# Kernel tuning notes

Hardware: AMD Instinct MI355X
Metric: run time of the kernel (lower is better)

## Reference

```python
import jax, jax.numpy as jnp
import numpy as np

DIM = 384
HEADS = 12
AGENT = 49
POOL = 7  # int(sqrt(AGENT))


def setup_inputs() -> dict:
    key = jax.random.key(0)
    ks = jax.random.split(key, 9)
    b, c, h, w = 32, DIM, 56, 56
    x = jax.random.normal(ks[0], (b, c, h, w), dtype=jnp.float32)
    qkv_w = jax.random.normal(ks[1], (c, 3 * c), dtype=jnp.float32) * 0.02
    qkv_b = jnp.zeros((3 * c,), dtype=jnp.float32)
    proj_w = jax.random.normal(ks[2], (c, c), dtype=jnp.float32) * 0.02
    proj_b = jnp.zeros((c,), dtype=jnp.float32)
    an_bias = jax.random.normal(ks[3], (HEADS, AGENT, 7, 7), dtype=jnp.float32) * 0.02
    na_bias = jax.random.normal(ks[4], (HEADS, AGENT, 7, 7), dtype=jnp.float32) * 0.02
    dwc_w = jax.random.normal(ks[5], (c, 1, 3, 3), dtype=jnp.float32) * 0.1
    dwc_b = jnp.zeros((c,), dtype=jnp.float32)
    return {"x": x, "qkv_w": qkv_w, "qkv_b": qkv_b, "proj_w": proj_w,
            "proj_b": proj_b, "an_bias": an_bias, "na_bias": na_bias,
            "dwc_w": dwc_w, "dwc_b": dwc_b}


def agent_attention(x, qkv_w, qkv_b, proj_w, proj_b, an_bias, na_bias, dwc_w, dwc_b):
    b, c, h, w = x.shape
    n = h * w
    H = HEADS
    hd = c // H
    scale = hd ** -0.5

    shortcut = x
    xf = x.reshape(b, c, n).transpose(0, 2, 1)            # [b, n, c]
    qkv = xf @ qkv_w + qkv_b                              # [b, n, 3c]
    q, k, v = jnp.split(qkv, 3, axis=-1)                  # each [b, n, c]

    # agent tokens: adaptive avg pool of q over uniform (h//POOL, w//POOL) windows
    q_img = q.reshape(b, h, w, c)
    agent = q_img.reshape(b, POOL, h // POOL, POOL, w // POOL, c).mean(axis=(2, 4))
    agent = agent.reshape(b, AGENT, c)

    # split heads -> [b, H, n, hd] / [b, H, AGENT, hd]
    qh = q.reshape(b, n, H, hd).transpose(0, 2, 1, 3)
    kh = k.reshape(b, n, H, hd).transpose(0, 2, 1, 3)
    vh = v.reshape(b, n, H, hd).transpose(0, 2, 1, 3)
    ah = agent.reshape(b, AGENT, H, hd).transpose(0, 2, 1, 3)

    # stage 1: agent tokens attend to keys (pos bias bilinearly upsampled 7x7 -> h x w)
    pb1 = jax.image.resize(an_bias, (H, AGENT, h, w), method='bilinear')
    pb1 = pb1.reshape(1, H, AGENT, n)
    agent_attn = jax.nn.softmax(
        jnp.einsum('bhad,bhnd->bhan', ah * scale, kh) + pb1, axis=-1)
    agent_v = jnp.einsum('bhan,bhnd->bhad', agent_attn, vh)  # [b, H, AGENT, hd]

    # stage 2: queries attend to agent tokens
    ab1 = jax.image.resize(na_bias, (H, AGENT, h, w), method='bilinear')
    ab1 = ab1.reshape(1, H, AGENT, n).transpose(0, 1, 3, 2)  # [1, H, n, AGENT]
    q_attn = jax.nn.softmax(
        jnp.einsum('bhnd,bhad->bhna', qh * scale, ah) + ab1, axis=-1)
    o = jnp.einsum('bhna,bhad->bhnd', q_attn, agent_v)       # [b, H, n, hd]
    o = o.transpose(0, 2, 1, 3).reshape(b, n, c)

    # depthwise 3x3 conv on v (NCHW), residual add
    v_img = v.reshape(b, h, w, c).transpose(0, 3, 1, 2)      # [b, c, h, w]
    dw = jax.lax.conv_general_dilated(
        v_img, dwc_w, window_strides=(1, 1), padding='SAME',
        feature_group_count=c, dimension_numbers=('NCHW', 'OIHW', 'NCHW'))
    dw = dw + dwc_b[None, :, None, None]
    o = o + dw.transpose(0, 2, 3, 1).reshape(b, n, c)

    o = o @ proj_w + proj_b                                  # [b, n, c]
    o = o.reshape(b, h, w, c).transpose(0, 3, 1, 2)          # [b, c, h, w]
    return shortcut * jax.nn.sigmoid(o)


def reference(x, qkv_w, qkv_b, proj_w, proj_b, an_bias, na_bias, dwc_w, dwc_b):
    return agent_attention(x, qkv_w, qkv_b, proj_w, proj_b,
                           an_bias, na_bias, dwc_w, dwc_b)
```

## Files before the change

### kernel.cpp

```cpp
#include <hip/hip_runtime.h>

#define DIM    384
#define HEADS  12
#define NPIX   3136
#define BATCH  32
#define AGENTS 49
#define HD     32

typedef unsigned short u16;
typedef unsigned int   u32;
typedef __attribute__((ext_vector_type(8))) short short8;
typedef __attribute__((ext_vector_type(4))) float f32x4;

__device__ __forceinline__ float bf2f(u16 u) { return __uint_as_float(((u32)u) << 16); }
__device__ __forceinline__ u16 f2bf(float f) {
    u32 i = __float_as_uint(f);
    u32 r = i + 0x7fffu + ((i >> 16) & 1u);
    return (u16)(r >> 16);
}

__device__ __forceinline__ void unpack_row32(const u16* p, float* f) {
    const uint4* q = (const uint4*)p;
#pragma unroll
    for (int i = 0; i < 4; i++) {
        uint4 u = q[i];
        u32 w0 = u.x, w1 = u.y, w2 = u.z, w3 = u.w;
        f[i*8+0] = __uint_as_float(w0 << 16); f[i*8+1] = __uint_as_float(w0 & 0xffff0000u);
        f[i*8+2] = __uint_as_float(w1 << 16); f[i*8+3] = __uint_as_float(w1 & 0xffff0000u);
        f[i*8+4] = __uint_as_float(w2 << 16); f[i*8+5] = __uint_as_float(w2 & 0xffff0000u);
        f[i*8+6] = __uint_as_float(w3 << 16); f[i*8+7] = __uint_as_float(w3 & 0xffff0000u);
    }
}

__global__ __launch_bounds__(256) void transpose_mat(const float* __restrict__ src, u16* __restrict__ dst,
                                                     int R, int C) {
    __shared__ u16 tile[64][65];
    int c0 = blockIdx.x * 64, r0 = blockIdx.y * 64;
    int t0 = threadIdx.x & 63, t1 = threadIdx.x >> 6;
#pragma unroll
    for (int i = 0; i < 16; i++) {
        int r = t1 + i*4;
        tile[t0][r] = f2bf(src[(size_t)(r0 + r)*C + c0 + t0]);
    }
    __syncthreads();
#pragma unroll
    for (int i = 0; i < 16; i++) {
        int c = t1 + i*4;
        dst[(size_t)(c0 + c)*R + r0 + t0] = tile[c][t0];
    }
}

__global__ __launch_bounds__(256) void upsample_bias(const float* __restrict__ src, float* __restrict__ dst) {
    int idx = blockIdx.x * 256 + threadIdx.x;
    int xo = idx % 56; int t = idx / 56;
    int yo = t % 56;   int ha = t / 56;
    float fy = yo * 0.125f - 0.4375f;
    float fx = xo * 0.125f - 0.4375f;
    float y0f = floorf(fy), x0f = floorf(fx);
    float wy = fy - y0f, wx = fx - x0f;
    int y0 = (int)y0f, x0 = (int)x0f;
    int y0c = max(y0, 0), y1c = min(y0 + 1, 6);
    int x0c = max(x0, 0), x1c = min(x0 + 1, 6);
    const float* sp = src + (size_t)ha * 49;
    float v00 = sp[y0c*7 + x0c], v01 = sp[y0c*7 + x1c];
    float v10 = sp[y1c*7 + x0c], v11 = sp[y1c*7 + x1c];
    dst[idx] = (1.f-wy)*((1.f-wx)*v00 + wx*v01) + wy*((1.f-wx)*v10 + wx*v11);
}

__global__ __launch_bounds__(256) void zero_init(float* __restrict__ p, int n) {
    int i = blockIdx.x * 256 + threadIdx.x;
    if (i < n) p[i] = 0.f;
}

__device__ __forceinline__ void mfma_tile(const short* As, const short* Bs, f32x4 acc[4][4],
                                          int wm, int wn, int quad, int lr) {
#pragma unroll
    for (int ks = 0; ks < 2; ks++) {
        int g = ks*4 + quad;
        short8 af[4], bg[4];
#pragma unroll
        for (int im = 0; im < 4; im++) {
            int r = wm*64 + im*16 + lr;
            af[im] = *(const short8*)&As[r*64 + ((g ^ (r & 7)) << 3)];
        }
#pragma unroll
        for (int in_ = 0; in_ < 4; in_++) {
            int r = wn*64 + in_*16 + lr;
            bg[in_] = *(const short8*)&Bs[r*64 + ((g ^ (r & 7)) << 3)];
        }
#pragma unroll
        for (int im = 0; im < 4; im++)
#pragma unroll
            for (int in_ = 0; in_ < 4; in_++)
                acc[im][in_] = __builtin_amdgcn_mfma_f32_16x16x32_bf16(af[im], bg[in_], acc[im][in_], 0, 0, 0);
    }
}

__global__ __launch_bounds__(256) void gemm_qkv(const float* __restrict__ x, const u16* __restrict__ Bw,
                                                const float* __restrict__ bias,
                                                u16* __restrict__ qb, u16* __restrict__ kb, u16* __restrict__ vb) {
    __shared__ __align__(16) short As[128*64];
    __shared__ __align__(16) short Bs[128*64];
    f32x4 acc[4][4] = {};
    const int n0 = blockIdx.x * 128;
    const int p0 = blockIdx.y * 128;
    const int bb = blockIdx.z;
    const int tid  = threadIdx.x;
    const int lane = tid & 63, wave = tid >> 6;
    const int wm = wave >> 1, wn = wave & 1;
    const int quad = lane >> 4, lr = lane & 15;
    const int ch_ = tid >> 2;
    const int seg = tid & 3;
    const int pbase = seg * 32;
    const bool segok = (p0 + pbase) < NPIX;

    for (int kt = 0; kt < DIM; kt += 64) {
        __syncthreads();
        u16 vals[32];
        if (segok) {
            const float4* xp = (const float4*)(x + ((size_t)bb*DIM + kt + ch_)*NPIX + p0 + pbase);
#pragma unroll
            for (int j = 0; j < 8; j++) {
                float4 u = xp[j];
                vals[j*4+0] = f2bf(u.x); vals[j*4+1] = f2bf(u.y);
                vals[j*4+2] = f2bf(u.z); vals[j*4+3] = f2bf(u.w);
            }
        } else {
#pragma unroll
            for (int i = 0; i < 32; i++) vals[i] = 0;
        }
#pragma unroll
        for (int i = 0; i < 32; i++) {
            int r = pbase + i;
            As[r*64 + (((ch_ >> 3) ^ (i & 7)) << 3) + (ch_ & 7)] = (short)vals[i];
        }
#pragma unroll
        for (int c2 = 0; c2 < 4; c2++) {
            int idx = c2*256 + tid;
            int r = idx >> 3, g = idx & 7;
            int so = r*64 + ((g ^ (r & 7)) << 3);
            *(uint4*)&Bs[so] = *(const uint4*)&Bw[(size_t)(n0 + r)*DIM + kt + g*8];
        }
        __syncthreads();
        mfma_tile(As, Bs, acc, wm, wn, quad, lr);
    }
#pragma unroll
    for (int in_ = 0; in_ < 4; in_++) {
        int col = n0 + wn*64 + in_*16 + lr;
        int which = col / 384;
        int ch = col - which*384;
        int head = ch >> 5, d = ch & 31;
        float bcol = bias[col];
        u16* dstp = (which == 0) ? qb : ((which == 1) ? kb : vb);
#pragma unroll
        for (int im = 0; im < 4; im++) {
            int prow = p0 + wm*64 + im*16 + quad*4;
#pragma unroll
            for (int r = 0; r < 4; r++) {
                int pix = prow + r;
                if (pix < NPIX) {
                    float v = acc[im][in_][r] + bcol;
                    dstp[((size_t)(bb*HEADS + head)*NPIX + pix)*HD + d] = f2bf(v);
                }
            }
        }
    }
}

__global__ __launch_bounds__(256) void gemm_proj(const u16* __restrict__ A, const u16* __restrict__ Bw,
                                                 const float* __restrict__ bias, const float* __restrict__ xin,
                                                 float* __restrict__ outp) {
    __shared__ __align__(16) short As[128*64];
    __shared__ __align__(16) short Bs[128*64];
    f32x4 acc[4][4] = {};
    const int n0 = blockIdx.x * 128, m0 = blockIdx.y * 128;
    const int tid  = threadIdx.x;
    const int lane = tid & 63, wave = tid >> 6;
    const int wm = wave >> 1, wn = wave & 1;
    const int quad = lane >> 4, lr = lane & 15;
    for (int kt = 0; kt < DIM; kt += 64) {
        __syncthreads();
#pragma unroll
        for (int c = 0; c < 4; c++) {
            int idx = c*256 + tid;
            int r = idx >> 3, g = idx & 7;
            int so = r*64 + ((g ^ (r & 7)) << 3);
            *(uint4*)&As[so] = *(const uint4*)&A[(size_t)(m0 + r)*DIM + kt + g*8];
            *(uint4*)&Bs[so] = *(const uint4*)&Bw[(size_t)(n0 + r)*DIM + kt + g*8];
        }
        __syncthreads();
        mfma_tile(As, Bs, acc, wm, wn, quad, lr);
    }
#pragma unroll
    for (int in_ = 0; in_ < 4; in_++) {
        int col = n0 + wn*64 + in_*16 + lr;
        float bcol = bias[col];
#pragma unroll
        for (int im = 0; im < 4; im++) {
            int rowb = m0 + wm*64 + im*16 + quad*4;
#pragma unroll
            for (int r = 0; r < 4; r++) {
                int grow = rowb + r;
                int bb = grow / NPIX;
                int pix = grow - bb*NPIX;
                float o = acc[im][in_][r] + bcol;
                float sg = 1.f / (1.f + __expf(-o));
                size_t xi = ((size_t)bb*DIM + col)*NPIX + pix;
                outp[xi] = xin[xi] * sg;
            }
        }
    }
}

__global__ __launch_bounds__(256) void pool_q(const u16* __restrict__ qb, float* __restrict__ agent) {
    int gt = blockIdx.x * 256 + threadIdx.x;
    int d = gt & 31;
    int t2 = gt >> 5;
    int a = t2 % 49;
    int bh = t2 / 49;
    int ay = a / 7, ax = a % 7;
    const u16* qp = qb + (size_t)bh*NPIX*HD + d;
    float s = 0.f;
#pragma unroll
    for (int dy = 0; dy < 8; dy++)
#pragma unroll
        for (int dx = 0; dx < 8; dx++)
            s += bf2f(qp[(size_t)((ay*8 + dy)*56 + ax*8 + dx)*HD]);
    agent[gt] = s * (1.f/64.f);
}

#define S1_CHUNK  224
#define S1_NCHUNK 14
#define S1_PSTR   228

__global__ __launch_bounds__(256) void stage1_part(const u16* __restrict__ kb, const u16* __restrict__ vb,
                                                   const float* __restrict__ agent, const float* __restrict__ pb1,
                                                   float* __restrict__ accv, float* __restrict__ accl) {
    __shared__ __align__(16) float ah_s[AGENTS*HD];
    __shared__ __align__(16) float P_s[AGENTS*S1_PSTR];
    const int chunk = blockIdx.x;
    const int bh    = blockIdx.y;
    const int hh    = bh % HEADS;
    const int tid   = threadIdx.x;
    const int pix0  = chunk * S1_CHUNK;
    const float scale = 0.1767766952966369f;

    for (int i = tid; i < AGENTS*HD; i += 256)
        ah_s[i] = agent[(size_t)bh*AGENTS*HD + i];
    __syncthreads();

    if (tid < S1_CHUNK) {
        float kf[32];
        unpack_row32(kb + ((size_t)bh*NPIX + pix0 + tid)*HD, kf);
        const float* pbp = pb1 + (size_t)hh*AGENTS*NPIX + pix0 + tid;
        for (int a = 0; a < AGENTS; a++) {
            const float* ap = &ah_s[a*HD];
            float s0 = 0.f, s1 = 0.f, s2 = 0.f, s3 = 0.f;
#pragma unroll
            for (int d = 0; d < 32; d += 4) {
                s0 = fmaf(ap[d+0], kf[d+0], s0);
                s1 = fmaf(ap[d+1], kf[d+1], s1);
                s2 = fmaf(ap[d+2], kf[d+2], s2);
                s3 = fmaf(ap[d+3], kf[d+3], s3);
            }
            float s = ((s0+s1)+(s2+s3))*scale + pbp[(size_t)a*NPIX];
            P_s[a*S1_PSTR + tid] = __expf(s);
        }
    }
    __syncthreads();

    if (tid < 196) {
        int a = tid >> 2, sub = tid & 3;
        const float* pp = &P_s[a*S1_PSTR + sub*56];
        float ls = 0.f;
        for (int k = 0; k < 56; k++) ls += pp[k];
        ls += __shfl_xor(ls, 1, 64);
        ls += __shfl_xor(ls, 2, 64);
        if (sub == 0) atomicAdd(&accl[(size_t)bh*AGENTS + a], ls);
    }

    const int d = tid & 31, g = tid >> 5;
    float acc[AGENTS];
#pragma unroll
    for (int a = 0; a < AGENTS; a++) acc[a] = 0.f;
    const u16* vp = vb + ((size_t)bh*NPIX + pix0)*HD + d;
    for (int p8 = 0; p8 < 7; p8++) {
        int pixl = p8*32 + g*4;
        float v0 = bf2f(vp[(size_t)(pixl+0)*HD]);
        float v1 = bf2f(vp[(size_t)(pixl+1)*HD]);
        float v2 = bf2f(vp[(size_t)(pixl+2)*HD]);
        float v3 = bf2f(vp[(size_t)(pixl+3)*HD]);
#pragma unroll
        for (int a = 0; a < AGENTS; a++) {
            f32x4 pq = *(const f32x4*)&P_s[a*S1_PSTR + pixl];
            acc[a] = fmaf(pq[0], v0, fmaf(pq[1], v1, fmaf(pq[2], v2, fmaf(pq[3], v3, acc[a]))));
        }
    }
    __syncthreads();

#pragma unroll
    for (int a = 0; a < AGENTS; a++) acc[a] += __shfl_xor(acc[a], 32, 64);
    float* red = (float*)P_s;
    const int w = tid >> 6;
    if ((tid & 63) < 32) {
#pragma unroll
        for (int a = 0; a < AGENTS; a++) red[(w*AGENTS + a)*HD + d] = acc[a];
    }
    __syncthreads();
    for (int i = tid; i < AGENTS*HD; i += 256) {
        float s = red[i] + red[AGENTS*HD + i] + red[2*AGENTS*HD + i] + red[3*AGENTS*HD + i];
        atomicAdd(&accv[(size_t)bh*AGENTS*HD + i], s);
    }
}

__global__ __launch_bounds__(256) void stage1_final(const float* __restrict__ accv, const float* __restrict__ accl,
                                                    float* __restrict__ agentv) {
    int i = blockIdx.x * 256 + threadIdx.x;
    agentv[i] = accv[i] / accl[i >> 5];
}

__global__ __launch_bounds__(256) void stage2(const u16* __restrict__ qb, const float* __restrict__ agent,
                                              const float* __restrict__ agentv, const float* __restrict__ ab1,
                                              u16* __restrict__ obuf) {
    __shared__ float ah_s[AGENTS*32];
    __shared__ float av_s[AGENTS*32];
    const int b = blockIdx.z, hh = blockIdx.y, chunk = blockIdx.x;
    const int bh = b*HEADS + hh;
    for (int i = threadIdx.x; i < AGENTS*32; i += 256) {
        ah_s[i] = agent[(size_t)bh*AGENTS*HD + i];
        av_s[i] = agentv[(size_t)bh*AGENTS*HD + i];
    }
    __syncthreads();
    int pix = chunk*256 + threadIdx.x;
    if (pix >= NPIX) return;
    const float scale = 0.1767766952966369f;
    float qf[32];
    unpack_row32(qb + ((size_t)bh*NPIX + pix)*HD, qf);
    float oacc[32];
#pragma unroll
    for (int d = 0; d < 32; d++) oacc[d] = 0.f;
    float l = 0.f;
    const float* abp = ab1 + (size_t)hh*AGENTS*NPIX + pix;
    for (int a = 0; a < AGENTS; a++) {
        float s = 0.f;
#pragma unroll
        for (int d = 0; d < 32; d++) s = fmaf(qf[d], ah_s[a*32 + d], s);
        s = s * scale + abp[(size_t)a*NPIX];
        float p = __expf(s);
        l += p;
#pragma unroll
        for (int d = 0; d < 32; d++) oacc[d] = fmaf(p, av_s[a*32 + d], oacc[d]);
    }
    float inv = 1.f / l;
    u16* op = obuf + ((size_t)b*NPIX + pix)*DIM + hh*HD;
#pragma unroll
    for (int d2 = 0; d2 < 16; d2++) {
        u32 lo = f2bf(oacc[2*d2] * inv);
        u32 hi = f2bf(oacc[2*d2 + 1] * inv);
        ((u32*)op)[d2] = lo | (hi << 16);
    }
}

__global__ __launch_bounds__(256) void dwconv_add(const u16* __restrict__ vb, const float* __restrict__ dwcw,
                                                  const float* __restrict__ dwcb, u16* __restrict__ obuf) {
    const int chunk = blockIdx.x;
    const int hh = blockIdx.y, b = blockIdx.z;
    const int dd = threadIdx.x & 31, pg = threadIdx.x >> 5;
    const int ch = hh*HD + dd;
    float wgt[9];
#pragma unroll
    for (int i = 0; i < 9; i++) wgt[i] = dwcw[ch*9 + i];
    float bbias = dwcb[ch];
    const u16* vp = vb + (size_t)(b*HEADS + hh)*NPIX*HD + dd;
#pragma unroll
    for (int i = 0; i < 4; i++) {
        int pix = chunk*32 + i*8 + pg;
        int y = pix / 56, x0 = pix - y*56;
        float s = bbias;
#pragma unroll
        for (int dy = 0; dy < 3; dy++) {
            int yy = y + dy - 1;
            if (yy < 0 || yy > 55) continue;
#pragma unroll
            for (int dx = 0; dx < 3; dx++) {
                int xx = x0 + dx - 1;
                if (xx < 0 || xx > 55) continue;
                s = fmaf(wgt[dy*3 + dx], bf2f(vp[(size_t)(yy*56 + xx)*HD]), s);
            }
        }
        size_t oi = ((size_t)b*NPIX + pix)*DIM + ch;
        obuf[oi] = f2bf(bf2f(obuf[oi]) + s);
    }
}

extern "C" void kernel_launch(void* const* d_in, const int* in_sizes, int n_in,
                              void* d_out, int out_size, void* d_ws, size_t ws_size,
                              hipStream_t stream) {
    const float* x     = (const float*)d_in[0];
    const float* qkvw  = (const float*)d_in[1];
    const float* qkvb  = (const float*)d_in[2];
    const float* projw = (const float*)d_in[3];
    const float* projb = (const float*)d_in[4];
    const float* anb   = (const float*)d_in[5];
    const float* nab   = (const float*)d_in[6];
    const float* dwcw  = (const float*)d_in[7];
    const float* dwcb  = (const float*)d_in[8];
    float* out = (float*)d_out;

    char* w = (char*)d_ws;
    const size_t SZ_BNC = (size_t)BATCH*NPIX*DIM*2;
    u16* qb     = (u16*)w;  w += SZ_BNC;
    u16* kb     = (u16*)w;  w += SZ_BNC;
    u16* vb     = (u16*)w;  w += SZ_BNC;
    u16* qkvwT  = (u16*)w;  w += (size_t)1152*384*2;
    u16* projwT = (u16*)w;  w += (size_t)384*384*2;
    u16* obuf   = kb;

    char* o = (char*)d_out;
    float* pb1    = (float*)o; o += (size_t)HEADS*AGENTS*NPIX*4;
    float* ab1    = (float*)o; o += (size_t)HEADS*AGENTS*NPIX*4;
    float* agent  = (float*)o; o += (size_t)BATCH*HEADS*AGENTS*HD*4;
    float* agentv = (float*)o; o += (size_t)BATCH*HEADS*AGENTS*HD*4;
    float* accv   = (float*)o; o += (size_t)BATCH*HEADS*AGENTS*HD*4;
    float* accl   = (float*)o; o += (size_t)BATCH*HEADS*AGENTS*4;

    const int nacc = BATCH*HEADS*AGENTS*(HD + 1);

    transpose_mat<<<dim3(18, 6),     256, 0, stream>>>(qkvw, qkvwT, 384, 1152);
    transpose_mat<<<dim3(6, 6),      256, 0, stream>>>(projw, projwT, 384, 384);
    upsample_bias<<<dim3(7203),      256, 0, stream>>>(anb, pb1);
    upsample_bias<<<dim3(7203),      256, 0, stream>>>(nab, ab1);
    zero_init    <<<dim3((nacc + 255)/256), 256, 0, stream>>>(accv, nacc);
    gemm_qkv     <<<dim3(9, 25, 32), 256, 0, stream>>>(x, qkvwT, qkvb, qb, kb, vb);
    pool_q       <<<dim3(2352),      256, 0, stream>>>(qb, agent);
    stage1_part  <<<dim3(S1_NCHUNK, BATCH*HEADS), 256, 0, stream>>>(kb, vb, agent, pb1, accv, accl);
    stage1_final <<<dim3(2352),      256, 0, stream>>>(accv, accl, agentv);
    stage2       <<<dim3(13, 12, 32),256, 0, stream>>>(qb, agent, agentv, ab1, obuf);
    dwconv_add   <<<dim3(98, 12, 32),256, 0, stream>>>(vb, dwcw, dwcb, obuf);
    gemm_proj    <<<dim3(3, 784),    256, 0, stream>>>(obuf, projwT, projb, x, out);
}
```

Before: 1.424 ms.

## Pre-transpose x to bf16 row-major and swizzle GEMM block order

```diff
diff --git a/kernel.cpp b/kernel.cpp
--- a/kernel.cpp
+++ b/kernel.cpp
@@ -47,6 +47,31 @@
     for (int i = 0; i < 16; i++) {
         int c = t1 + i*4;
         dst[(size_t)(c0 + c)*R + r0 + t0] = tile[c][t0];
+    }
+}
+
+__global__ __launch_bounds__(256) void convert_x(const float* __restrict__ x, u16* __restrict__ xT) {
+    __shared__ float tile[64][65];
+    const int p0 = blockIdx.x * 64;
+    const int c0 = blockIdx.y * 64;
+    const int b  = blockIdx.z;
+    const int t0 = threadIdx.x & 63, t1 = threadIdx.x >> 6;
+#pragma unroll
+    for (int i = 0; i < 16; i++) {
+        int ch = t1 + i*4;
+        tile[t0][ch] = x[((size_t)b*DIM + c0 + ch)*NPIX + p0 + t0];
+    }
+    __syncthreads();
+    const int cb = threadIdx.x & 7, r = threadIdx.x >> 3;
+#pragma unroll
+    for (int half = 0; half < 2; half++) {
+        int rr = r + half*32;
+        const float* tp = &tile[rr][cb*8];
+        u32 w0 = f2bf(tp[0]) | ((u32)f2bf(tp[1]) << 16);
+        u32 w1 = f2bf(tp[2]) | ((u32)f2bf(tp[3]) << 16);
+        u32 w2 = f2bf(tp[4]) | ((u32)f2bf(tp[5]) << 16);
+        u32 w3 = f2bf(tp[6]) | ((u32)f2bf(tp[7]) << 16);
+        *(uint4*)&xT[((size_t)b*NPIX + p0 + rr)*DIM + c0 + cb*8] = make_uint4(w0, w1, w2, w3);
     }
 }
 
@@ -96,49 +121,32 @@
     }
 }
 
-__global__ __launch_bounds__(256) void gemm_qkv(const float* __restrict__ x, const u16* __restrict__ Bw,
+__global__ __launch_bounds__(256) void gemm_qkv(const u16* __restrict__ xT, const u16* __restrict__ Bw,
                                                 const float* __restrict__ bias,
                                                 u16* __restrict__ qb, u16* __restrict__ kb, u16* __restrict__ vb) {
     __shared__ __align__(16) short As[128*64];
     __shared__ __align__(16) short Bs[128*64];
     f32x4 acc[4][4] = {};
-    const int n0 = blockIdx.x * 128;
-    const int p0 = blockIdx.y * 128;
-    const int bb = blockIdx.z;
+    const int l  = blockIdx.x + 9*(blockIdx.y + 25*blockIdx.z);
+    const int k8 = l & 7, j = l >> 3;
+    const int c  = (j/9)*8 + k8;
+    const int i9 = j - (j/9)*9;
+    const int n0 = i9 * 128;
+    const int p0 = (c % 25) * 128;
+    const int bb = c / 25;
     const int tid  = threadIdx.x;
     const int lane = tid & 63, wave = tid >> 6;
     const int wm = wave >> 1, wn = wave & 1;
     const int quad = lane >> 4, lr = lane & 15;
-    const int ch_ = tid >> 2;
-    const int seg = tid & 3;
-    const int pbase = seg * 32;
-    const bool segok = (p0 + pbase) < NPIX;
 
     for (int kt = 0; kt < DIM; kt += 64) {
         __syncthreads();
-        u16 vals[32];
-        if (segok) {
-            const float4* xp = (const float4*)(x + ((size_t)bb*DIM + kt + ch_)*NPIX + p0 + pbase);
-#pragma unroll
-            for (int j = 0; j < 8; j++) {
-                float4 u = xp[j];
-                vals[j*4+0] = f2bf(u.x); vals[j*4+1] = f2bf(u.y);
-                vals[j*4+2] = f2bf(u.z); vals[j*4+3] = f2bf(u.w);
-            }
-        } else {
-#pragma unroll
-            for (int i = 0; i < 32; i++) vals[i] = 0;
-        }
-#pragma unroll
-        for (int i = 0; i < 32; i++) {
-            int r = pbase + i;
-            As[r*64 + (((ch_ >> 3) ^ (i & 7)) << 3) + (ch_ & 7)] = (short)vals[i];
-        }
 #pragma unroll
         for (int c2 = 0; c2 < 4; c2++) {
             int idx = c2*256 + tid;
             int r = idx >> 3, g = idx & 7;
             int so = r*64 + ((g ^ (r & 7)) << 3);
+            *(uint4*)&As[so] = *(const uint4*)&xT[((size_t)bb*NPIX + p0 + r)*DIM + kt + g*8];
             *(uint4*)&Bs[so] = *(const uint4*)&Bw[(size_t)(n0 + r)*DIM + kt + g*8];
         }
         __syncthreads();
@@ -173,7 +181,11 @@
     __shared__ __align__(16) short As[128*64];
     __shared__ __align__(16) short Bs[128*64];
     f32x4 acc[4][4] = {};
-    const int n0 = blockIdx.x * 128, m0 = blockIdx.y * 128;
+    const int l  = blockIdx.x + 3*blockIdx.y;
+    const int k8 = l & 7, j = l >> 3;
+    const int c  = (j/3)*8 + k8;
+    const int i3 = j - (j/3)*3;
+    const int n0 = i3*128, m0 = c*128;
     const int tid  = threadIdx.x;
     const int lane = tid & 63, wave = tid >> 6;
     const int wm = wave >> 1, wn = wave & 1;
@@ -181,8 +193,8 @@
     for (int kt = 0; kt < DIM; kt += 64) {
         __syncthreads();
 #pragma unroll
-        for (int c = 0; c < 4; c++) {
-            int idx = c*256 + tid;
+        for (int c2 = 0; c2 < 4; c2++) {
+            int idx = c2*256 + tid;
             int r = idx >> 3, g = idx & 7;
             int so = r*64 + ((g ^ (r & 7)) << 3);
             *(uint4*)&As[so] = *(const uint4*)&A[(size_t)(m0 + r)*DIM + kt + g*8];
@@ -423,15 +435,17 @@
     float* agentv = (float*)o; o += (size_t)BATCH*HEADS*AGENTS*HD*4;
     float* accv   = (float*)o; o += (size_t)BATCH*HEADS*AGENTS*HD*4;
     float* accl   = (float*)o; o += (size_t)BATCH*HEADS*AGENTS*4;
+    u16*   xT     = (u16*)o;   o += SZ_BNC;
 
     const int nacc = BATCH*HEADS*AGENTS*(HD + 1);
 
+    convert_x    <<<dim3(49, 6, 32), 256, 0, stream>>>(x, xT);
     transpose_mat<<<dim3(18, 6),     256, 0, stream>>>(qkvw, qkvwT, 384, 1152);
     transpose_mat<<<dim3(6, 6),      256, 0, stream>>>(projw, projwT, 384, 384);
     upsample_bias<<<dim3(7203),      256, 0, stream>>>(anb, pb1);
     upsample_bias<<<dim3(7203),      256, 0, stream>>>(nab, ab1);
     zero_init    <<<dim3((nacc + 255)/256), 256, 0, stream>>>(accv, nacc);
-    gemm_qkv     <<<dim3(9, 25, 32), 256, 0, stream>>>(x, qkvwT, qkvb, qb, kb, vb);
+    gemm_qkv     <<<dim3(9, 25, 32), 256, 0, stream>>>(xT, qkvwT, qkvb, qb, kb, vb);
     pool_q       <<<dim3(2352),      256, 0, stream>>>(qb, agent);
     stage1_part  <<<dim3(S1_NCHUNK, BATCH*HEADS), 256, 0, stream>>>(kb, vb, agent, pb1, accv, accl);
     stage1_final <<<dim3(2352),      256, 0, stream>>>(accv, accl, agentv);
```

Measured after the change: 1.360 ms. 1.05x faster.
